# Kernel tuning notes

Measured on AMD Instinct MI355X. Metric: run time of the kernel, lower is better.

## Reference

```python
import jax, jax.numpy as jnp
import numpy as np

# ---- static config ----
B, D, H, W, C = 4, 8, 56, 56, 192
Md, Mh, Mw = 2, 7, 7
Sd, Sh, Sw = 1, 3, 3
NH = 6
HD = C // NH
SCALE = HD ** -0.5
N = Md * Mh * Mw  # 98
NW = (D // Md) * (H // Mh) * (W // Mw)  # 256 windows per batch element


def _rel_pos_index():
    coords = np.stack(np.meshgrid(np.arange(Md), np.arange(Mh), np.arange(Mw), indexing='ij'))
    cf = coords.reshape(3, -1)
    rc = (cf[:, :, None] - cf[:, None, :]).transpose(1, 2, 0)
    rc[..., 0] += Md - 1
    rc[..., 1] += Mh - 1
    rc[..., 2] += Mw - 1
    rc[..., 0] *= (2 * Mh - 1) * (2 * Mw - 1)
    rc[..., 1] *= 2 * Mw - 1
    return rc.sum(-1)  # (N, N) int

REL_IDX = jnp.asarray(_rel_pos_index())


def _build_attn_mask():
    img = np.zeros((D, H, W), dtype=np.float32)
    cnt = 0
    for ds in (slice(0, -Md), slice(-Md, -Sd), slice(-Sd, None)):
        for hs in (slice(0, -Mh), slice(-Mh, -Sh), slice(-Sh, None)):
            for ws in (slice(0, -Mw), slice(-Mw, -Sw), slice(-Sw, None)):
                img[ds, hs, ws] = cnt
                cnt += 1
    mw = img.reshape(D // Md, Md, H // Mh, Mh, W // Mw, Mw)
    mw = mw.transpose(0, 2, 4, 1, 3, 5).reshape(-1, N)  # (NW, N)
    am = mw[:, None, :] - mw[:, :, None]
    return np.where(am != 0, -100.0, 0.0).astype(np.float32)  # (NW, N, N)


def window_partition(x):  # (B, D, H, W, C) -> (B*NW, N, C)
    x = x.reshape(B, D // Md, Md, H // Mh, Mh, W // Mw, Mw, C)
    return x.transpose(0, 1, 3, 5, 2, 4, 6, 7).reshape(-1, N, C)


def window_reverse(w):  # (B*NW, N, C) -> (B, D, H, W, C)
    x = w.reshape(B, D // Md, H // Mh, W // Mw, Md, Mh, Mw, C)
    return x.transpose(0, 1, 4, 2, 5, 3, 6, 7).reshape(B, D, H, W, C)


def layer_norm(x, g, b, eps=1e-5):
    mu = x.mean(-1, keepdims=True)
    var = ((x - mu) ** 2).mean(-1, keepdims=True)
    return (x - mu) * jax.lax.rsqrt(var + eps) * g + b


def setup_inputs() -> dict:
    key = jax.random.key(0)
    ks = jax.random.split(key, 6)
    return {
        'x': jax.random.normal(ks[0], (B, D * H * W, C), jnp.float32),
        'attn_mask': jnp.asarray(_build_attn_mask()),
        'norm1_g': jnp.ones((C,), jnp.float32),
        'norm1_b': jnp.zeros((C,), jnp.float32),
        'qkv_w': jax.random.normal(ks[1], (3 * C, C), jnp.float32) * 0.02,
        'qkv_b': jnp.zeros((3 * C,), jnp.float32),
        'rel_bias': jax.random.normal(ks[2], ((2 * Md - 1) * (2 * Mh - 1) * (2 * Mw - 1), NH), jnp.float32) * 0.02,
        'proj_w': jax.random.normal(ks[3], (C, C), jnp.float32) * 0.02,
        'proj_b': jnp.zeros((C,), jnp.float32),
        'fc1_w': jax.random.normal(ks[4], (C, C), jnp.float32) * 0.02,
        'fc1_b': jnp.zeros((C,), jnp.float32),
    }


def reference(x, attn_mask, norm1_g, norm1_b, qkv_w, qkv_b, rel_bias, proj_w, proj_b, fc1_w, fc1_b):
    shortcut = x
    h = layer_norm(x, norm1_g, norm1_b).reshape(B, D, H, W, C)
    # cyclic shift (dims divisible by window -> no padding needed)
    h = jnp.roll(h, shift=(-Sd, -Sh, -Sw), axis=(1, 2, 3))
    xw = window_partition(h)  # (B*NW, N, C)
    B_ = xw.shape[0]
    qkv = (xw @ qkv_w.T + qkv_b).reshape(B_, N, 3, NH, HD).transpose(2, 0, 3, 1, 4)
    q, k, v = qkv[0], qkv[1], qkv[2]  # (B_, NH, N, HD)
    attn = jnp.einsum('bhnd,bhmd->bhnm', q * SCALE, k)
    bias = rel_bias[REL_IDX.reshape(-1)].reshape(N, N, NH).transpose(2, 0, 1)  # (NH, N, N)
    attn = attn + bias[None]
    # additive shift mask per window
    attn = attn.reshape(B, NW, NH, N, N) + attn_mask[None, :, None]
    attn = jax.nn.softmax(attn.reshape(B_, NH, N, N), axis=-1)
    out = jnp.einsum('bhnm,bhmd->bhnd', attn, v).transpose(0, 2, 1, 3).reshape(B_, N, C)
    out = out @ proj_w.T + proj_b
    h = window_reverse(out)
    h = jnp.roll(h, shift=(Sd, Sh, Sw), axis=(1, 2, 3)).reshape(B, D * H * W, C)
    h = jax.nn.gelu(h @ fc1_w.T + fc1_b, approximate=False)
    return shortcut + h
```

## Files before the change

### kernel.cpp

```cpp
#include <hip/hip_runtime.h>
#include <cstdint>
#include <cstddef>

typedef __bf16 bf16_t;
typedef __bf16 bf16x8 __attribute__((ext_vector_type(8)));
typedef float  f32x4  __attribute__((ext_vector_type(4)));

#define DHW   25088
#define SCALE 0.17677669529663687f

__device__ inline f32x4 mfma16(bf16x8 a, bf16x8 b, f32x4 c) {
  return __builtin_amdgcn_mfma_f32_16x16x32_bf16(a, b, c, 0, 0, 0);
}

__device__ inline size_t wrow_to_grow(int orow) {
  int win = orow / 98, tok = orow % 98;
  int b = win >> 8, wr = win & 255;
  int bd = wr >> 6, bh = (wr >> 3) & 7, bwi = wr & 7;
  int md = tok / 49, mh = (tok / 7) % 7, mw = tok % 7;
  int d = (bd * 2 + md + 1) & 7;
  int h = bh * 7 + mh + 3; if (h >= 56) h -= 56;
  int w = bwi * 7 + mw + 3; if (w >= 56) w -= 56;
  return (size_t)b * DHW + (size_t)((d * 56 + h) * 56 + w);
}

__global__ __launch_bounds__(256) void prep_all_kernel(
    const float* __restrict__ qkv_w, const float* __restrict__ proj_w,
    const float* __restrict__ fc1_w, const float* __restrict__ rel_bias,
    const float* __restrict__ mask,
    bf16_t* __restrict__ wq, bf16_t* __restrict__ wp, bf16_t* __restrict__ wf,
    bf16_t* __restrict__ bmr)
{
  int idx = blockIdx.x * 256 + threadIdx.x;
  if (idx < 110592) { wq[idx] = (bf16_t)qkv_w[idx]; return; }
  idx -= 110592;
  if (idx < 36864) { wp[idx] = (bf16_t)proj_w[idx]; return; }
  idx -= 36864;
  if (idx < 36864) { wf[idx] = (bf16_t)fc1_w[idx]; return; }
  idx -= 36864;
  if (idx >= 688128) return;
  int e    = idx & 31;
  int lane = (idx >> 5) & 63;
  int t2   = idx >> 11;
  int mt   = t2 % 7;
  int wh   = t2 / 7;
  int type = wh / 6, h = wh - type * 6;
  int winb = ((type & 4) ? 3 : 0) * 64 + ((type & 2) ? 7 : 0) * 8 + ((type & 1) ? 7 : 0);
  int g = lane >> 4, li = lane & 15;
  int nt2 = e >> 2, v = e & 3;
  int row = mt * 16 + g * 4 + v;
  int col = nt2 * 16 + li;
  float val = -1e30f;
  if (row < 98 && col < 98 && nt2 < 7) {
    int di = row / 49 - col / 49 + 1;
    int hi = (row / 7) % 7 - (col / 7) % 7 + 6;
    int wi = row % 7 - col % 7 + 6;
    int rid = di * 169 + hi * 13 + wi;
    val = mask[winb * 9604 + row * 98 + col] + rel_bias[rid * 6 + h];
  }
  bmr[idx] = (bf16_t)val;
}

__global__ __launch_bounds__(896) void fused_kernel(
    const float* __restrict__ x, const float* __restrict__ gw,
    const float* __restrict__ bw_, const bf16_t* __restrict__ wq,
    const float* __restrict__ qkv_b, const bf16_t* __restrict__ wp,
    const float* __restrict__ proj_b, const bf16_t* __restrict__ wf,
    const float* __restrict__ fc1_b, const bf16_t* __restrict__ bmr,
    float* __restrict__ out)
{
  __shared__ __align__(16) char smem[158528];
  bf16_t* U  = (bf16_t*)smem;
  bf16_t* Qs = (bf16_t*)(smem + 25600);
  bf16_t* Ks = (bf16_t*)(smem + 64800);
  bf16_t* Vt = (bf16_t*)(smem + 104000);
  float*  qb = (float*)(smem + 156224);
  float* gwb = (float*)smem;

  #define BS(r, c)     U[(r) * 200 + (c)]
  #define PSc(w, r, c) U[(w) * 640 + (r) * 40 + (c)]
  #define QS(r, c)     Qs[(r) * 200 + (c)]
  #define KS(r, c)     Ks[(r) * 200 + (c)]
  #define VT(d, t)     Vt[(d) * 136 + (t)]

  int win  = blockIdx.x;
  int winb = win & 255;
  int type = (((winb >> 6) == 3) ? 4 : 0) | ((((winb >> 3) & 7) == 7) ? 2 : 0)
           | (((winb & 7) == 7) ? 1 : 0);
  int tid  = threadIdx.x;
  int wid  = tid >> 6, lane = tid & 63;
  int wn = wid & 1, wm = wid >> 1;
  int g = lane >> 4, li = lane & 15;

  if (tid < 192) { gwb[tid] = gw[tid]; gwb[192 + tid] = bw_[tid]; }
  if (tid < 576) qb[tid] = qkv_b[tid];
  if (tid < 768) {
    uint4 z = {0u, 0u, 0u, 0u};
    int d = tid >> 2, part = tid & 3;
    *(uint4*)&VT(d, 96 + part * 8) = z;
  }

  int r = wm * 16 + li;
  float v[48];
  if (r < 98) {
    size_t growr = wrow_to_grow(win * 98 + r);
    const float* xr = x + growr * 192 + g * 8;
    #pragma unroll
    for (int ks = 0; ks < 6; ks++) {
      *(float4*)&v[ks * 8]     = *(const float4*)(xr + ks * 32);
      *(float4*)&v[ks * 8 + 4] = *(const float4*)(xr + ks * 32 + 4);
    }
  } else {
    #pragma unroll
    for (int i = 0; i < 48; i++) v[i] = 0.f;
  }
  float s = 0.f, sq = 0.f;
  #pragma unroll
  for (int i = 0; i < 48; i++) { s += v[i]; sq += v[i] * v[i]; }
  s += __shfl_xor(s, 16, 64); sq += __shfl_xor(sq, 16, 64);
  s += __shfl_xor(s, 32, 64); sq += __shfl_xor(sq, 32, 64);
  float mu   = s * (1.0f / 192.0f);
  float var  = sq * (1.0f / 192.0f) - mu * mu;
  float rstd = rsqrtf(var + 1e-5f);
  __syncthreads();
  bf16x8 afr[6];
  #pragma unroll
  for (int ks = 0; ks < 6; ks++) {
    bf16x8 t;
    #pragma unroll
    for (int j = 0; j < 8; j++) {
      int c = ks * 32 + g * 8 + j;
      t[j] = (r < 98) ? (bf16_t)((v[ks * 8 + j] - mu) * rstd * gwb[c] + gwb[192 + c])
                      : (bf16_t)0.0f;
    }
    afr[ks] = t;
  }

  uint4 st[2];
  #pragma unroll
  for (int i = 0; i < 2; i++) {
    int c = tid + 896 * i;
    if (c < 1536) {
      int rr = c / 24, ck = c % 24;
      st[i] = *(const uint4*)(wq + (size_t)rr * 192 + ck * 8);
    }
  }
  for (int nt = 0; nt < 9; nt++) {
    __syncthreads();
    #pragma unroll
    for (int i = 0; i < 2; i++) {
      int c = tid + 896 * i;
      if (c < 1536) {
        int rr = c / 24, ck = c % 24;
        *(uint4*)&BS(rr, ck * 8) = st[i];
      }
    }
    __syncthreads();
    if (nt < 8) {
      #pragma unroll
      for (int i = 0; i < 2; i++) {
        int c = tid + 896 * i;
        if (c < 1536) {
          int rr = c / 24, ck = c % 24;
          st[i] = *(const uint4*)(wq + (size_t)(nt + 1) * 12288 + (size_t)rr * 192 + ck * 8);
        }
      }
    }
    f32x4 acc[2] = {};
    #pragma unroll
    for (int ks = 0; ks < 6; ks++) {
      bf16x8 a = afr[ks];
      #pragma unroll
      for (int nl = 0; nl < 2; nl++) {
        bf16x8 b = *(const bf16x8*)&BS((wn * 2 + nl) * 16 + li, ks * 32 + g * 8);
        acc[nl] = mfma16(a, b, acc[nl]);
      }
    }
    #pragma unroll
    for (int nl = 0; nl < 2; nl++)
    #pragma unroll
    for (int vv = 0; vv < 4; vv++) {
      int row = wm * 16 + g * 4 + vv;
      if (row < 98) {
        int col = nt * 64 + (wn * 2 + nl) * 16 + li;
        float val = acc[nl][vv] + qb[col];
        if (nt < 3)      QS(row, col)       = (bf16_t)(val * SCALE);
        else if (nt < 6) KS(row, col - 192) = (bf16_t)val;
        else             VT(col - 384, row) = (bf16_t)val;
      }
    }
  }
  __syncthreads();

  int mt  = wm;
  int rq  = mt * 16 + li;
  int rqc = rq < 98 ? rq : 97;
  for (int hh = 0; hh < 3; hh++) {
    int h = wn * 3 + hh;
    const bf16_t* bmp = bmr + ((((size_t)(type * 6 + h)) * 7 + mt) * 64 + lane) * 32;
    bf16x8 bm0 = *(const bf16x8*)(bmp);
    bf16x8 bm1 = *(const bf16x8*)(bmp + 8);
    bf16x8 bm2 = *(const bf16x8*)(bmp + 16);
    bf16x8 bm3 = *(const bf16x8*)(bmp + 24);
    bf16x8 af = *(const bf16x8*)&QS(rqc, h * 32 + g * 8);
    float logit[7][4];
    #pragma unroll
    for (int nt2 = 0; nt2 < 7; nt2++) {
      int rk = nt2 * 16 + li;
      int rkc = rk < 98 ? rk : 97;
      bf16x8 bfr = *(const bf16x8*)&KS(rkc, h * 32 + g * 8);
      f32x4 z = {};
      f32x4 S = mfma16(af, bfr, z);
      #pragma unroll
      for (int vv = 0; vv < 4; vv++) {
        int e = nt2 * 4 + vv;
        float bmv = (e < 8) ? (float)bm0[e] : (e < 16) ? (float)bm1[e - 8]
                  : (e < 24) ? (float)bm2[e - 16] : (float)bm3[e - 24];
        logit[nt2][vv] = S[vv] + bmv;
      }
    }
    #pragma unroll
    for (int vv = 0; vv < 4; vv++) {
      float mx = logit[0][vv];
      #pragma unroll
      for (int nt2 = 1; nt2 < 7; nt2++) mx = fmaxf(mx, logit[nt2][vv]);
      #pragma unroll
      for (int off = 1; off < 16; off <<= 1) mx = fmaxf(mx, __shfl_xor(mx, off, 64));
      float se = 0.f;
      #pragma unroll
      for (int nt2 = 0; nt2 < 7; nt2++) {
        float p = __expf(logit[nt2][vv] - mx);
        logit[nt2][vv] = p; se += p;
      }
      #pragma unroll
      for (int off = 1; off < 16; off <<= 1) se += __shfl_xor(se, off, 64);
      float inv = 1.0f / se;
      #pragma unroll
      for (int nt2 = 0; nt2 < 7; nt2++) logit[nt2][vv] *= inv;
    }
    f32x4 o0 = {}, o1 = {};
    #pragma unroll
    for (int ch = 0; ch < 4; ch++) {
      #pragma unroll
      for (int nl = 0; nl < 2; nl++) {
        int nt2 = ch * 2 + nl;
        #pragma unroll
        for (int vv = 0; vv < 4; vv++) {
          bf16_t pv = (nt2 < 7) ? (bf16_t)logit[nt2][vv] : (bf16_t)0.0f;
          PSc(wid, g * 4 + vv, nl * 16 + li) = pv;
        }
      }
      bf16x8 pf = *(const bf16x8*)&PSc(wid, li, g * 8);
      bf16x8 v0 = *(const bf16x8*)&VT(h * 32 + li, ch * 32 + g * 8);
      bf16x8 v1 = *(const bf16x8*)&VT(h * 32 + 16 + li, ch * 32 + g * 8);
      o0 = mfma16(pf, v0, o0);
      o1 = mfma16(pf, v1, o1);
    }
    #pragma unroll
    for (int vv = 0; vv < 4; vv++) {
      int row = mt * 16 + g * 4 + vv;
      if (row < 98) {
        QS(row, h * 32 + li)      = (bf16_t)o0[vv];
        QS(row, h * 32 + 16 + li) = (bf16_t)o1[vv];
      }
    }
  }
  __syncthreads();

  float* bfb = qb;
  if (tid < 192) bfb[tid] = proj_b[tid];
  bf16x8 a2[6];
  #pragma unroll
  for (int ks = 0; ks < 6; ks++)
    a2[ks] = *(const bf16x8*)&QS(rqc, ks * 32 + g * 8);
  #pragma unroll
  for (int i = 0; i < 2; i++) {
    int c = tid + 896 * i;
    if (c < 1536) {
      int rr = c / 24, ck = c % 24;
      st[i] = *(const uint4*)(wp + (size_t)rr * 192 + ck * 8);
    }
  }
  for (int nt = 0; nt < 3; nt++) {
    __syncthreads();
    #pragma unroll
    for (int i = 0; i < 2; i++) {
      int c = tid + 896 * i;
      if (c < 1536) {
        int rr = c / 24, ck = c % 24;
        *(uint4*)&BS(rr, ck * 8) = st[i];
      }
    }
    __syncthreads();
    if (nt < 2) {
      #pragma unroll
      for (int i = 0; i < 2; i++) {
        int c = tid + 896 * i;
        if (c < 1536) {
          int rr = c / 24, ck = c % 24;
          st[i] = *(const uint4*)(wp + (size_t)(nt + 1) * 12288 + (size_t)rr * 192 + ck * 8);
        }
      }
    }
    f32x4 acc[2] = {};
    #pragma unroll
    for (int ks = 0; ks < 6; ks++) {
      bf16x8 a = a2[ks];
      #pragma unroll
      for (int nl = 0; nl < 2; nl++) {
        bf16x8 b = *(const bf16x8*)&BS((wn * 2 + nl) * 16 + li, ks * 32 + g * 8);
        acc[nl] = mfma16(a, b, acc[nl]);
      }
    }
    #pragma unroll
    for (int nl = 0; nl < 2; nl++)
    #pragma unroll
    for (int vv = 0; vv < 4; vv++) {
      int row = wm * 16 + g * 4 + vv;
      if (row < 98) {
        int col = nt * 64 + (wn * 2 + nl) * 16 + li;
        KS(row, col) = (bf16_t)(acc[nl][vv] + bfb[col]);
      }
    }
  }
  __syncthreads();

  if (tid < 192) bfb[tid] = fc1_b[tid];
  bf16x8 a3[6];
  #pragma unroll
  for (int ks = 0; ks < 6; ks++)
    a3[ks] = *(const bf16x8*)&KS(rqc, ks * 32 + g * 8);
  #pragma unroll
  for (int i = 0; i < 2; i++) {
    int c = tid + 896 * i;
    if (c < 1536) {
      int rr = c / 24, ck = c % 24;
      st[i] = *(const uint4*)(wf + (size_t)rr * 192 + ck * 8);
    }
  }
  size_t growv[4];
  #pragma unroll
  for (int vv = 0; vv < 4; vv++) {
    int row = wm * 16 + g * 4 + vv;
    growv[vv] = (row < 98) ? wrow_to_grow(win * 98 + row) : (size_t)0;
  }
  for (int nt = 0; nt < 3; nt++) {
    __syncthreads();
    #pragma unroll
    for (int i = 0; i < 2; i++) {
      int c = tid + 896 * i;
      if (c < 1536) {
        int rr = c / 24, ck = c % 24;
        *(uint4*)&BS(rr, ck * 8) = st[i];
      }
    }
    __syncthreads();
    if (nt < 2) {
      #pragma unroll
      for (int i = 0; i < 2; i++) {
        int c = tid + 896 * i;
        if (c < 1536) {
          int rr = c / 24, ck = c % 24;
          st[i] = *(const uint4*)(wf + (size_t)(nt + 1) * 12288 + (size_t)rr * 192 + ck * 8);
        }
      }
    }
    f32x4 acc[2] = {};
    #pragma unroll
    for (int ks = 0; ks < 6; ks++) {
      bf16x8 a = a3[ks];
      #pragma unroll
      for (int nl = 0; nl < 2; nl++) {
        bf16x8 b = *(const bf16x8*)&BS((wn * 2 + nl) * 16 + li, ks * 32 + g * 8);
        acc[nl] = mfma16(a, b, acc[nl]);
      }
    }
    #pragma unroll
    for (int vv = 0; vv < 4; vv++) {
      int row = wm * 16 + g * 4 + vv;
      if (row < 98) {
        const float* xr = x + growv[vv] * 192;
        float* op = out + growv[vv] * 192;
        #pragma unroll
        for (int nl = 0; nl < 2; nl++) {
          int col = nt * 64 + (wn * 2 + nl) * 16 + li;
          float val = acc[nl][vv] + bfb[col];
          float ge = 0.5f * val * (1.0f + erff(val * 0.70710678118654752f));
          op[col] = xr[col] + ge;
        }
      }
    }
  }
  #undef BS
  #undef PSc
  #undef QS
  #undef KS
  #undef VT
}

extern "C" void kernel_launch(void* const* d_in, const int* in_sizes, int n_in,
                              void* d_out, int out_size, void* d_ws, size_t ws_size,
                              hipStream_t stream) {
  (void)in_sizes; (void)n_in; (void)out_size; (void)ws_size;
  const float* x         = (const float*)d_in[0];
  const float* attn_mask = (const float*)d_in[1];
  const float* n1g       = (const float*)d_in[2];
  const float* n1b       = (const float*)d_in[3];
  const float* qkv_w     = (const float*)d_in[4];
  const float* qkv_b     = (const float*)d_in[5];
  const float* rel_bias  = (const float*)d_in[6];
  const float* proj_w    = (const float*)d_in[7];
  const float* proj_b    = (const float*)d_in[8];
  const float* fc1_w     = (const float*)d_in[9];
  const float* fc1_b     = (const float*)d_in[10];
  float* out = (float*)d_out;

  char* ws = (char*)d_ws;
  size_t off = 0;
  auto alloc = [&](size_t bytes) -> char* {
    char* p = ws + off;
    off += (bytes + 255) & ~(size_t)255;
    return p;
  };
  bf16_t* wq  = (bf16_t*)alloc(110592 * 2);
  bf16_t* wp  = (bf16_t*)alloc(36864 * 2);
  bf16_t* wf  = (bf16_t*)alloc(36864 * 2);
  bf16_t* bmr = (bf16_t*)alloc((size_t)688128 * 2);

  prep_all_kernel<<<3408, 256, 0, stream>>>(qkv_w, proj_w, fc1_w, rel_bias,
                                            attn_mask, wq, wp, wf, bmr);
  fused_kernel<<<1024, 896, 0, stream>>>(x, n1g, n1b, wq, qkv_b, wp, proj_b,
                                         wf, fc1_b, bmr, out);
}
```

Measured before the change: 387.0 us.

## Interleave QKV projection with per-head-pair attention to shrink LDS footprint

Restructures the fused Swin block kernel so that QKV is computed two heads at a time, with attention run for that pair right after, instead of materializing full Q/K/V for all heads. Shared memory drops from about 158KB to about 79KB, which could allow two workgroups per CU. Register pressure is also lowered: LayerNorm inputs are re-read from global rather than held in 48 registers, logits are packed as fp16 pairs, and launch bounds gain a minimum-occupancy hint. The costs are recomputing the LayerNorm fragments three times, extra syncs per head pair, and fp16 rounding of logits before softmax.

```diff
diff --git a/kernel.cpp b/kernel.cpp
--- a/kernel.cpp
+++ b/kernel.cpp
@@ -4,13 +4,27 @@
 
 typedef __bf16 bf16_t;
 typedef __bf16 bf16x8 __attribute__((ext_vector_type(8)));
+typedef __bf16 bf16x4 __attribute__((ext_vector_type(4)));
 typedef float  f32x4  __attribute__((ext_vector_type(4)));
+typedef _Float16 f16_t;
 
 #define DHW   25088
 #define SCALE 0.17677669529663687f
 
 __device__ inline f32x4 mfma16(bf16x8 a, bf16x8 b, f32x4 c) {
   return __builtin_amdgcn_mfma_f32_16x16x32_bf16(a, b, c, 0, 0, 0);
+}
+
+__device__ inline unsigned pkh(float a, float b) {
+  unsigned short ua = __builtin_bit_cast(unsigned short, (f16_t)a);
+  unsigned short ub = __builtin_bit_cast(unsigned short, (f16_t)b);
+  return (unsigned)ua | ((unsigned)ub << 16);
+}
+__device__ inline float upklo(unsigned u) {
+  return (float)__builtin_bit_cast(f16_t, (unsigned short)(u & 0xffffu));
+}
+__device__ inline float upkhi(unsigned u) {
+  return (float)__builtin_bit_cast(f16_t, (unsigned short)(u >> 16));
 }
 
 __device__ inline size_t wrow_to_grow(int orow) {
@@ -61,7 +75,7 @@
   bmr[idx] = (bf16_t)val;
 }
 
-__global__ __launch_bounds__(896) void fused_kernel(
+__global__ __launch_bounds__(896, 7) void fused_kernel(
     const float* __restrict__ x, const float* __restrict__ gw,
     const float* __restrict__ bw_, const bf16_t* __restrict__ wq,
     const float* __restrict__ qkv_b, const bf16_t* __restrict__ wp,
@@ -69,19 +83,22 @@
     const float* __restrict__ fc1_b, const bf16_t* __restrict__ bmr,
     float* __restrict__ out)
 {
-  __shared__ __align__(16) char smem[158528];
-  bf16_t* U  = (bf16_t*)smem;
-  bf16_t* Qs = (bf16_t*)(smem + 25600);
-  bf16_t* Ks = (bf16_t*)(smem + 64800);
-  bf16_t* Vt = (bf16_t*)(smem + 104000);
-  float*  qb = (float*)(smem + 156224);
-  float* gwb = (float*)smem;
+  __shared__ __align__(16) char smem[79104];
+  bf16_t* U   = (bf16_t*)smem;
+  bf16_t* Qh  = (bf16_t*)(smem + 25600);
+  bf16_t* Kh  = (bf16_t*)(smem + 41728);
+  bf16_t* Vt  = (bf16_t*)(smem + 57856);
+  bf16_t* AoS = (bf16_t*)(smem + 25600);
+  bf16_t* C1  = (bf16_t*)(smem + 25600);
+  float*  qb  = (float*)(smem + 75264);
+  float*  gwb = (float*)(smem + 77568);
 
   #define BS(r, c)     U[(r) * 200 + (c)]
   #define PSc(w, r, c) U[(w) * 640 + (r) * 40 + (c)]
-  #define QS(r, c)     Qs[(r) * 200 + (c)]
-  #define KS(r, c)     Ks[(r) * 200 + (c)]
+  #define QH(r, c)     Qh[(r) * 72 + (c)]
+  #define KH(r, c)     Kh[(r) * 72 + (c)]
   #define VT(d, t)     Vt[(d) * 136 + (t)]
+  #define C1M(r, c)    C1[(r) * 200 + (c)]
 
   int win  = blockIdx.x;
   int winb = win & 255;
@@ -94,59 +111,76 @@
 
   if (tid < 192) { gwb[tid] = gw[tid]; gwb[192 + tid] = bw_[tid]; }
   if (tid < 576) qb[tid] = qkv_b[tid];
-  if (tid < 768) {
+  {
     uint4 z = {0u, 0u, 0u, 0u};
-    int d = tid >> 2, part = tid & 3;
-    *(uint4*)&VT(d, 96 + part * 8) = z;
+    for (int c = tid; c < 1088; c += 896) ((uint4*)Vt)[c] = z;
   }
 
   int r = wm * 16 + li;
-  float v[48];
+  const float* xr = nullptr;
   if (r < 98) {
     size_t growr = wrow_to_grow(win * 98 + r);
-    const float* xr = x + growr * 192 + g * 8;
+    xr = x + growr * 192 + g * 8;
+  }
+  float mu, rstd;
+  {
+    float s = 0.f, sq = 0.f;
+    if (xr) {
+      #pragma unroll
+      for (int ks = 0; ks < 6; ks++) {
+        float4 a = *(const float4*)(xr + ks * 32);
+        float4 b = *(const float4*)(xr + ks * 32 + 4);
+        s += a.x + a.y + a.z + a.w + b.x + b.y + b.z + b.w;
+        sq += a.x*a.x + a.y*a.y + a.z*a.z + a.w*a.w
+            + b.x*b.x + b.y*b.y + b.z*b.z + b.w*b.w;
+      }
+    }
+    s += __shfl_xor(s, 16, 64); sq += __shfl_xor(sq, 16, 64);
+    s += __shfl_xor(s, 32, 64); sq += __shfl_xor(sq, 32, 64);
+    mu = s * (1.0f / 192.0f);
+    float var = sq * (1.0f / 192.0f) - mu * mu;
+    rstd = rsqrtf(var + 1e-5f);
+  }
+  __syncthreads();
+
+  auto build_afr = [&](bf16x8* afr) {
     #pragma unroll
     for (int ks = 0; ks < 6; ks++) {
-      *(float4*)&v[ks * 8]     = *(const float4*)(xr + ks * 32);
-      *(float4*)&v[ks * 8 + 4] = *(const float4*)(xr + ks * 32 + 4);
-    }
-  } else {
-    #pragma unroll
-    for (int i = 0; i < 48; i++) v[i] = 0.f;
-  }
-  float s = 0.f, sq = 0.f;
-  #pragma unroll
-  for (int i = 0; i < 48; i++) { s += v[i]; sq += v[i] * v[i]; }
-  s += __shfl_xor(s, 16, 64); sq += __shfl_xor(sq, 16, 64);
-  s += __shfl_xor(s, 32, 64); sq += __shfl_xor(sq, 32, 64);
-  float mu   = s * (1.0f / 192.0f);
-  float var  = sq * (1.0f / 192.0f) - mu * mu;
-  float rstd = rsqrtf(var + 1e-5f);
-  __syncthreads();
-  bf16x8 afr[6];
-  #pragma unroll
-  for (int ks = 0; ks < 6; ks++) {
-    bf16x8 t;
-    #pragma unroll
-    for (int j = 0; j < 8; j++) {
-      int c = ks * 32 + g * 8 + j;
-      t[j] = (r < 98) ? (bf16_t)((v[ks * 8 + j] - mu) * rstd * gwb[c] + gwb[192 + c])
-                      : (bf16_t)0.0f;
-    }
-    afr[ks] = t;
-  }
+      bf16x8 t;
+      if (xr) {
+        int c0 = ks * 32 + g * 8;
+        float4 a = *(const float4*)(xr + ks * 32);
+        float4 b = *(const float4*)(xr + ks * 32 + 4);
+        float4 ga = *(const float4*)&gwb[c0],      gb = *(const float4*)&gwb[c0 + 4];
+        float4 ba = *(const float4*)&gwb[192 + c0], bb = *(const float4*)&gwb[192 + c0 + 4];
+        t[0] = (bf16_t)((a.x - mu) * rstd * ga.x + ba.x);
+        t[1] = (bf16_t)((a.y - mu) * rstd * ga.y + ba.y);
+        t[2] = (bf16_t)((a.z - mu) * rstd * ga.z + ba.z);
+        t[3] = (bf16_t)((a.w - mu) * rstd * ga.w + ba.w);
+        t[4] = (bf16_t)((b.x - mu) * rstd * gb.x + bb.x);
+        t[5] = (bf16_t)((b.y - mu) * rstd * gb.y + bb.y);
+        t[6] = (bf16_t)((b.z - mu) * rstd * gb.z + bb.z);
+        t[7] = (bf16_t)((b.w - mu) * rstd * gb.w + bb.w);
+      } else {
+        #pragma unroll
+        for (int j = 0; j < 8; j++) t[j] = (bf16_t)0.0f;
+      }
+      afr[ks] = t;
+    }
+  };
 
   uint4 st[2];
-  #pragma unroll
-  for (int i = 0; i < 2; i++) {
-    int c = tid + 896 * i;
-    if (c < 1536) {
-      int rr = c / 24, ck = c % 24;
-      st[i] = *(const uint4*)(wq + (size_t)rr * 192 + ck * 8);
-    }
-  }
-  for (int nt = 0; nt < 9; nt++) {
-    __syncthreads();
+  auto loadw = [&](const bf16_t* w, int tile) {
+    #pragma unroll
+    for (int i = 0; i < 2; i++) {
+      int c = tid + 896 * i;
+      if (c < 1536) {
+        int rr = c / 24, ck = c % 24;
+        st[i] = *(const uint4*)(w + (size_t)tile * 12288 + (size_t)rr * 192 + ck * 8);
+      }
+    }
+  };
+  auto storebs = [&]() {
     #pragma unroll
     for (int i = 0; i < 2; i++) {
       int c = tid + 896 * i;
@@ -155,26 +189,154 @@
         *(uint4*)&BS(rr, ck * 8) = st[i];
       }
     }
+  };
+
+  int rqc = (wm * 16 + li < 98) ? (wm * 16 + li) : 97;
+  bf16x8 a2loc[3];
+
+  loadw(wq, 0);
+  #pragma unroll
+  for (int hp = 0; hp < 3; hp++) {
+    bf16x8 afr[6];
+    build_afr(afr);
+    for (int tp = 0; tp < 3; tp++) {
+      __syncthreads();
+      storebs();
+      __syncthreads();
+      if (tp < 2) loadw(wq, hp + 3 * (tp + 1));
+      f32x4 acc[2] = {};
+      #pragma unroll
+      for (int ks = 0; ks < 6; ks++) {
+        bf16x8 b0 = *(const bf16x8*)&BS((wn * 2 + 0) * 16 + li, ks * 32 + g * 8);
+        bf16x8 b1 = *(const bf16x8*)&BS((wn * 2 + 1) * 16 + li, ks * 32 + g * 8);
+        acc[0] = mfma16(afr[ks], b0, acc[0]);
+        acc[1] = mfma16(afr[ks], b1, acc[1]);
+      }
+      #pragma unroll
+      for (int nl = 0; nl < 2; nl++)
+      #pragma unroll
+      for (int vv = 0; vv < 4; vv++) {
+        int row = wm * 16 + g * 4 + vv;
+        if (row < 98) {
+          int cl = (wn * 2 + nl) * 16 + li;
+          float val = acc[nl][vv] + qb[tp * 192 + hp * 64 + cl];
+          if (tp == 0)      QH(row, cl) = (bf16_t)(val * SCALE);
+          else if (tp == 1) KH(row, cl) = (bf16_t)val;
+          else              VT(cl, row) = (bf16_t)val;
+        }
+      }
+    }
     __syncthreads();
-    if (nt < 8) {
-      #pragma unroll
-      for (int i = 0; i < 2; i++) {
-        int c = tid + 896 * i;
-        if (c < 1536) {
-          int rr = c / 24, ck = c % 24;
-          st[i] = *(const uint4*)(wq + (size_t)(nt + 1) * 12288 + (size_t)rr * 192 + ck * 8);
+
+    {
+      int h = 2 * hp + wn, hl = wn * 32;
+      const bf16_t* bmp = bmr + ((((size_t)(type * 6 + h)) * 7 + wm) * 64 + lane) * 32;
+      bf16x8 af = *(const bf16x8*)&QH(rqc, hl + g * 8);
+      unsigned lp[7][2];
+      float mx0 = -3.0e38f, mx1 = -3.0e38f, mx2 = -3.0e38f, mx3 = -3.0e38f;
+      #pragma unroll
+      for (int nt2 = 0; nt2 < 7; nt2++) {
+        int rk = nt2 * 16 + li;
+        int rkc = rk < 98 ? rk : 97;
+        bf16x8 kf = *(const bf16x8*)&KH(rkc, hl + g * 8);
+        f32x4 z = {};
+        f32x4 S = mfma16(af, kf, z);
+        bf16x4 bm4 = *(const bf16x4*)(bmp + nt2 * 4);
+        float l0 = S[0] + (float)bm4[0];
+        float l1 = S[1] + (float)bm4[1];
+        float l2 = S[2] + (float)bm4[2];
+        float l3 = S[3] + (float)bm4[3];
+        mx0 = fmaxf(mx0, l0); mx1 = fmaxf(mx1, l1);
+        mx2 = fmaxf(mx2, l2); mx3 = fmaxf(mx3, l3);
+        lp[nt2][0] = pkh(l0, l1);
+        lp[nt2][1] = pkh(l2, l3);
+      }
+      #pragma unroll
+      for (int off = 1; off < 16; off <<= 1) {
+        mx0 = fmaxf(mx0, __shfl_xor(mx0, off, 64));
+        mx1 = fmaxf(mx1, __shfl_xor(mx1, off, 64));
+        mx2 = fmaxf(mx2, __shfl_xor(mx2, off, 64));
+        mx3 = fmaxf(mx3, __shfl_xor(mx3, off, 64));
+      }
+      float se0 = 0.f, se1 = 0.f, se2 = 0.f, se3 = 0.f;
+      #pragma unroll
+      for (int nt2 = 0; nt2 < 7; nt2++) {
+        float p0 = __expf(upklo(lp[nt2][0]) - mx0);
+        float p1 = __expf(upkhi(lp[nt2][0]) - mx1);
+        float p2 = __expf(upklo(lp[nt2][1]) - mx2);
+        float p3 = __expf(upkhi(lp[nt2][1]) - mx3);
+        se0 += p0; se1 += p1; se2 += p2; se3 += p3;
+        lp[nt2][0] = pkh(p0, p1);
+        lp[nt2][1] = pkh(p2, p3);
+      }
+      #pragma unroll
+      for (int off = 1; off < 16; off <<= 1) {
+        se0 += __shfl_xor(se0, off, 64); se1 += __shfl_xor(se1, off, 64);
+        se2 += __shfl_xor(se2, off, 64); se3 += __shfl_xor(se3, off, 64);
+      }
+      float inv0 = 1.0f / se0, inv1 = 1.0f / se1;
+      float inv2 = 1.0f / se2, inv3 = 1.0f / se3;
+      f32x4 o0 = {}, o1 = {};
+      #pragma unroll
+      for (int ch = 0; ch < 4; ch++) {
+        #pragma unroll
+        for (int nl = 0; nl < 2; nl++) {
+          int nt2 = ch * 2 + nl;
+          if (nt2 < 7) {
+            PSc(wid, g * 4 + 0, nl * 16 + li) = (bf16_t)(upklo(lp[nt2][0]) * inv0);
+            PSc(wid, g * 4 + 1, nl * 16 + li) = (bf16_t)(upkhi(lp[nt2][0]) * inv1);
+            PSc(wid, g * 4 + 2, nl * 16 + li) = (bf16_t)(upklo(lp[nt2][1]) * inv2);
+            PSc(wid, g * 4 + 3, nl * 16 + li) = (bf16_t)(upkhi(lp[nt2][1]) * inv3);
+          } else {
+            PSc(wid, g * 4 + 0, nl * 16 + li) = (bf16_t)0.0f;
+            PSc(wid, g * 4 + 1, nl * 16 + li) = (bf16_t)0.0f;
+            PSc(wid, g * 4 + 2, nl * 16 + li) = (bf16_t)0.0f;
+            PSc(wid, g * 4 + 3, nl * 16 + li) = (bf16_t)0.0f;
+          }
         }
-      }
-    }
+        bf16x8 pf = *(const bf16x8*)&PSc(wid, li, g * 8);
+        bf16x8 v0 = *(const bf16x8*)&VT(hl + li, ch * 32 + g * 8);
+        bf16x8 v1 = *(const bf16x8*)&VT(hl + 16 + li, ch * 32 + g * 8);
+        o0 = mfma16(pf, v0, o0);
+        o1 = mfma16(pf, v1, o1);
+      }
+      #pragma unroll
+      for (int vv = 0; vv < 4; vv++) {
+        PSc(wid, g * 4 + vv, li)      = (bf16_t)o0[vv];
+        PSc(wid, g * 4 + vv, 16 + li) = (bf16_t)o1[vv];
+      }
+      a2loc[hp] = *(const bf16x8*)&PSc(wid, li, g * 8);
+    }
+    if (hp < 2) loadw(wq, hp + 1);
+    else        loadw(wp, 0);
+  }
+
+  __syncthreads();
+  #pragma unroll
+  for (int hp = 0; hp < 3; hp++) {
+    int ks = 2 * hp + wn;
+    *(bf16x8*)(AoS + (size_t)(wm * 6 + ks) * 512 + lane * 8) = a2loc[hp];
+  }
+  if (tid < 192) qb[tid] = proj_b[tid];
+  __syncthreads();
+  bf16x8 a2[6];
+  #pragma unroll
+  for (int ks = 0; ks < 6; ks++)
+    a2[ks] = *(const bf16x8*)(AoS + (size_t)(wm * 6 + ks) * 512 + lane * 8);
+
+  for (int tp = 0; tp < 3; tp++) {
+    __syncthreads();
+    storebs();
+    __syncthreads();
+    if (tp < 2) loadw(wp, tp + 1);
+    else        loadw(wf, 0);
     f32x4 acc[2] = {};
     #pragma unroll
     for (int ks = 0; ks < 6; ks++) {
-      bf16x8 a = afr[ks];
-      #pragma unroll
-      for (int nl = 0; nl < 2; nl++) {
-        bf16x8 b = *(const bf16x8*)&BS((wn * 2 + nl) * 16 + li, ks * 32 + g * 8);
-        acc[nl] = mfma16(a, b, acc[nl]);
-      }
+      bf16x8 b0 = *(const bf16x8*)&BS((wn * 2 + 0) * 16 + li, ks * 32 + g * 8);
+      bf16x8 b1 = *(const bf16x8*)&BS((wn * 2 + 1) * 16 + li, ks * 32 + g * 8);
+      acc[0] = mfma16(a2[ks], b0, acc[0]);
+      acc[1] = mfma16(a2[ks], b1, acc[1]);
     }
     #pragma unroll
     for (int nl = 0; nl < 2; nl++)
@@ -182,220 +344,60 @@
     for (int vv = 0; vv < 4; vv++) {
       int row = wm * 16 + g * 4 + vv;
       if (row < 98) {
-        int col = nt * 64 + (wn * 2 + nl) * 16 + li;
-        float val = acc[nl][vv] + qb[col];
-        if (nt < 3)      QS(row, col)       = (bf16_t)(val * SCALE);
-        else if (nt < 6) KS(row, col - 192) = (bf16_t)val;
-        else             VT(col - 384, row) = (bf16_t)val;
+        int cl = tp * 64 + (wn * 2 + nl) * 16 + li;
+        C1M(row, cl) = (bf16_t)(acc[nl][vv] + qb[cl]);
       }
     }
   }
   __syncthreads();
 
-  int mt  = wm;
-  int rq  = mt * 16 + li;
-  int rqc = rq < 98 ? rq : 97;
-  for (int hh = 0; hh < 3; hh++) {
-    int h = wn * 3 + hh;
-    const bf16_t* bmp = bmr + ((((size_t)(type * 6 + h)) * 7 + mt) * 64 + lane) * 32;
-    bf16x8 bm0 = *(const bf16x8*)(bmp);
-    bf16x8 bm1 = *(const bf16x8*)(bmp + 8);
-    bf16x8 bm2 = *(const bf16x8*)(bmp + 16);
-    bf16x8 bm3 = *(const bf16x8*)(bmp + 24);
-    bf16x8 af = *(const bf16x8*)&QS(rqc, h * 32 + g * 8);
-    float logit[7][4];
-    #pragma unroll
-    for (int nt2 = 0; nt2 < 7; nt2++) {
-      int rk = nt2 * 16 + li;
-      int rkc = rk < 98 ? rk : 97;
-      bf16x8 bfr = *(const bf16x8*)&KS(rkc, h * 32 + g * 8);
-      f32x4 z = {};
-      f32x4 S = mfma16(af, bfr, z);
-      #pragma unroll
-      for (int vv = 0; vv < 4; vv++) {
-        int e = nt2 * 4 + vv;
-        float bmv = (e < 8) ? (float)bm0[e] : (e < 16) ? (float)bm1[e - 8]
-                  : (e < 24) ? (float)bm2[e - 16] : (float)bm3[e - 24];
-        logit[nt2][vv] = S[vv] + bmv;
-      }
-    }
-    #pragma unroll
-    for (int vv = 0; vv < 4; vv++) {
-      float mx = logit[0][vv];
-      #pragma unroll
-      for (int nt2 = 1; nt2 < 7; nt2++) mx = fmaxf(mx, logit[nt2][vv]);
-      #pragma unroll
-      for (int off = 1; off < 16; off <<= 1) mx = fmaxf(mx, __shfl_xor(mx, off, 64));
-      float se = 0.f;
-      #pragma unroll
-      for (int nt2 = 0; nt2 < 7; nt2++) {
-        float p = __expf(logit[nt2][vv] - mx);
-        logit[nt2][vv] = p; se += p;
-      }
-      #pragma unroll
-      for (int off = 1; off < 16; off <<= 1) se += __shfl_xor(se, off, 64);
-      float inv = 1.0f / se;
-      #pragma unroll
-      for (int nt2 = 0; nt2 < 7; nt2++) logit[nt2][vv] *= inv;
-    }
-    f32x4 o0 = {}, o1 = {};
-    #pragma unroll
-    for (int ch = 0; ch < 4; ch++) {
-      #pragma unroll
-      for (int nl = 0; nl < 2; nl++) {
-        int nt2 = ch * 2 + nl;
-        #pragma unroll
-        for (int vv = 0; vv < 4; vv++) {
-          bf16_t pv = (nt2 < 7) ? (bf16_t)logit[nt2][vv] : (bf16_t)0.0f;
-          PSc(wid, g * 4 + vv, nl * 16 + li) = pv;
-        }
-      }
-      bf16x8 pf = *(const bf16x8*)&PSc(wid, li, g * 8);
-      bf16x8 v0 = *(const bf16x8*)&VT(h * 32 + li, ch * 32 + g * 8);
-      bf16x8 v1 = *(const bf16x8*)&VT(h * 32 + 16 + li, ch * 32 + g * 8);
-      o0 = mfma16(pf, v0, o0);
-      o1 = mfma16(pf, v1, o1);
-    }
-    #pragma unroll
-    for (int vv = 0; vv < 4; vv++) {
-      int row = mt * 16 + g * 4 + vv;
-      if (row < 98) {
-        QS(row, h * 32 + li)      = (bf16_t)o0[vv];
-        QS(row, h * 32 + 16 + li) = (bf16_t)o1[vv];
-      }
-    }
-  }
-  __syncthreads();
-
-  float* bfb = qb;
-  if (tid < 192) bfb[tid] = proj_b[tid];
-  bf16x8 a2[6];
-  #pragma unroll
-  for (int ks = 0; ks < 6; ks++)
-    a2[ks] = *(const bf16x8*)&QS(rqc, ks * 32 + g * 8);
-  #pragma unroll
-  for (int i = 0; i < 2; i++) {
-    int c = tid + 896 * i;
-    if (c < 1536) {
-      int rr = c / 24, ck = c % 24;
-      st[i] = *(const uint4*)(wp + (size_t)rr * 192 + ck * 8);
-    }
-  }
-  for (int nt = 0; nt < 3; nt++) {
-    __syncthreads();
-    #pragma unroll
-    for (int i = 0; i < 2; i++) {
-      int c = tid + 896 * i;
-      if (c < 1536) {
-        int rr = c / 24, ck = c % 24;
-        *(uint4*)&BS(rr, ck * 8) = st[i];
-      }
-    }
-    __syncthreads();
-    if (nt < 2) {
-      #pragma unroll
-      for (int i = 0; i < 2; i++) {
-        int c = tid + 896 * i;
-        if (c < 1536) {
-          int rr = c / 24, ck = c % 24;
-          st[i] = *(const uint4*)(wp + (size_t)(nt + 1) * 12288 + (size_t)rr * 192 + ck * 8);
-        }
-      }
-    }
-    f32x4 acc[2] = {};
-    #pragma unroll
-    for (int ks = 0; ks < 6; ks++) {
-      bf16x8 a = a2[ks];
-      #pragma unroll
-      for (int nl = 0; nl < 2; nl++) {
-        bf16x8 b = *(const bf16x8*)&BS((wn * 2 + nl) * 16 + li, ks * 32 + g * 8);
-        acc[nl] = mfma16(a, b, acc[nl]);
-      }
-    }
-    #pragma unroll
-    for (int nl = 0; nl < 2; nl++)
-    #pragma unroll
-    for (int vv = 0; vv < 4; vv++) {
-      int row = wm * 16 + g * 4 + vv;
-      if (row < 98) {
-        int col = nt * 64 + (wn * 2 + nl) * 16 + li;
-        KS(row, col) = (bf16_t)(acc[nl][vv] + bfb[col]);
-      }
-    }
-  }
-  __syncthreads();
-
-  if (tid < 192) bfb[tid] = fc1_b[tid];
   bf16x8 a3[6];
   #pragma unroll
   for (int ks = 0; ks < 6; ks++)
-    a3[ks] = *(const bf16x8*)&KS(rqc, ks * 32 + g * 8);
-  #pragma unroll
-  for (int i = 0; i < 2; i++) {
-    int c = tid + 896 * i;
-    if (c < 1536) {
-      int rr = c / 24, ck = c % 24;
-      st[i] = *(const uint4*)(wf + (size_t)rr * 192 + ck * 8);
-    }
-  }
+    a3[ks] = *(const bf16x8*)&C1M(rqc, ks * 32 + g * 8);
+  if (tid < 192) qb[tid] = fc1_b[tid];
   size_t growv[4];
   #pragma unroll
   for (int vv = 0; vv < 4; vv++) {
     int row = wm * 16 + g * 4 + vv;
     growv[vv] = (row < 98) ? wrow_to_grow(win * 98 + row) : (size_t)0;
   }
-  for (int nt = 0; nt < 3; nt++) {
+
+  for (int tp = 0; tp < 3; tp++) {
     __syncthreads();
-    #pragma unroll
-    for (int i = 0; i < 2; i++) {
-      int c = tid + 896 * i;
-      if (c < 1536) {
-        int rr = c / 24, ck = c % 24;
-        *(uint4*)&BS(rr, ck * 8) = st[i];
-      }
-    }
+    storebs();
     __syncthreads();
-    if (nt < 2) {
-      #pragma unroll
-      for (int i = 0; i < 2; i++) {
-        int c = tid + 896 * i;
-        if (c < 1536) {
-          int rr = c / 24, ck = c % 24;
-          st[i] = *(const uint4*)(wf + (size_t)(nt + 1) * 12288 + (size_t)rr * 192 + ck * 8);
-        }
-      }
-    }
+    if (tp < 2) loadw(wf, tp + 1);
     f32x4 acc[2] = {};
     #pragma unroll
     for (int ks = 0; ks < 6; ks++) {
-      bf16x8 a = a3[ks];
-      #pragma unroll
-      for (int nl = 0; nl < 2; nl++) {
-        bf16x8 b = *(const bf16x8*)&BS((wn * 2 + nl) * 16 + li, ks * 32 + g * 8);
-        acc[nl] = mfma16(a, b, acc[nl]);
-      }
+      bf16x8 b0 = *(const bf16x8*)&BS((wn * 2 + 0) * 16 + li, ks * 32 + g * 8);
+      bf16x8 b1 = *(const bf16x8*)&BS((wn * 2 + 1) * 16 + li, ks * 32 + g * 8);
+      acc[0] = mfma16(a3[ks], b0, acc[0]);
+      acc[1] = mfma16(a3[ks], b1, acc[1]);
     }
     #pragma unroll
     for (int vv = 0; vv < 4; vv++) {
       int row = wm * 16 + g * 4 + vv;
       if (row < 98) {
-        const float* xr = x + growv[vv] * 192;
+        const float* xrr = x + growv[vv] * 192;
         float* op = out + growv[vv] * 192;
         #pragma unroll
         for (int nl = 0; nl < 2; nl++) {
-          int col = nt * 64 + (wn * 2 + nl) * 16 + li;
-          float val = acc[nl][vv] + bfb[col];
+          int cl = tp * 64 + (wn * 2 + nl) * 16 + li;
+          float val = acc[nl][vv] + qb[cl];
           float ge = 0.5f * val * (1.0f + erff(val * 0.70710678118654752f));
-          op[col] = xr[col] + ge;
+          op[cl] = xrr[cl] + ge;
         }
       }
     }
   }
   #undef BS
   #undef PSc
-  #undef QS
-  #undef KS
+  #undef QH
+  #undef KH
   #undef VT
+  #undef C1M
 }
 
 extern "C" void kernel_launch(void* const* d_in, const int* in_sizes, int n_in,
```

Result: slower. 507.8 us (+31.2%).

## Load GEMM weight fragments directly from global memory instead of staging through LDS

Applied to the files above, without the earlier changes.

The QKV, proj and fc1 GEMMs no longer copy 64-row weight tiles into shared memory behind two __syncthreads per tile. Each wave now reads its B fragments straight from global memory, relying on L2/L1 because every block reads the same small weights. The proj and fc1 biases are preloaded into dedicated LDS buffers at kernel start, so the barriers before those GEMMs are no longer needed for bias staging. This removes many barriers and LDS round-trips and shrinks LDS use, but it exposes global-load latency inside the MFMA loops with no prefetch, and the 7 row-waves issue redundant loads of the same weights.

```diff
diff --git a/kernel.cpp b/kernel.cpp
--- a/kernel.cpp
+++ b/kernel.cpp
@@ -69,15 +69,16 @@
     const float* __restrict__ fc1_b, const bf16_t* __restrict__ bmr,
     float* __restrict__ out)
 {
-  __shared__ __align__(16) char smem[158528];
+  __shared__ __align__(16) char smem[152384];
   bf16_t* U  = (bf16_t*)smem;
-  bf16_t* Qs = (bf16_t*)(smem + 25600);
-  bf16_t* Ks = (bf16_t*)(smem + 64800);
-  bf16_t* Vt = (bf16_t*)(smem + 104000);
-  float*  qb = (float*)(smem + 156224);
+  bf16_t* Qs = (bf16_t*)(smem + 17920);
+  bf16_t* Ks = (bf16_t*)(smem + 57120);
+  bf16_t* Vt = (bf16_t*)(smem + 96320);
+  float*  qb = (float*)(smem + 148544);
+  float*  pbuf = (float*)(smem + 150848);
+  float*  fbuf = (float*)(smem + 151616);
   float* gwb = (float*)smem;
 
-  #define BS(r, c)     U[(r) * 200 + (c)]
   #define PSc(w, r, c) U[(w) * 640 + (r) * 40 + (c)]
   #define QS(r, c)     Qs[(r) * 200 + (c)]
   #define KS(r, c)     Ks[(r) * 200 + (c)]
@@ -94,6 +95,9 @@
 
   if (tid < 192) { gwb[tid] = gw[tid]; gwb[192 + tid] = bw_[tid]; }
   if (tid < 576) qb[tid] = qkv_b[tid];
+  if (tid >= 576 && tid < 768) pbuf[tid - 576] = proj_b[tid - 576];
+  if (tid >= 768 && tid < 896) fbuf[tid - 768] = fc1_b[tid - 768];
+  if (tid < 64) fbuf[128 + tid] = fc1_b[128 + tid];
   if (tid < 768) {
     uint4 z = {0u, 0u, 0u, 0u};
     int d = tid >> 2, part = tid & 3;
@@ -136,45 +140,16 @@
     afr[ks] = t;
   }
 
-  uint4 st[2];
-  #pragma unroll
-  for (int i = 0; i < 2; i++) {
-    int c = tid + 896 * i;
-    if (c < 1536) {
-      int rr = c / 24, ck = c % 24;
-      st[i] = *(const uint4*)(wq + (size_t)rr * 192 + ck * 8);
-    }
-  }
   for (int nt = 0; nt < 9; nt++) {
-    __syncthreads();
-    #pragma unroll
-    for (int i = 0; i < 2; i++) {
-      int c = tid + 896 * i;
-      if (c < 1536) {
-        int rr = c / 24, ck = c % 24;
-        *(uint4*)&BS(rr, ck * 8) = st[i];
-      }
-    }
-    __syncthreads();
-    if (nt < 8) {
-      #pragma unroll
-      for (int i = 0; i < 2; i++) {
-        int c = tid + 896 * i;
-        if (c < 1536) {
-          int rr = c / 24, ck = c % 24;
-          st[i] = *(const uint4*)(wq + (size_t)(nt + 1) * 12288 + (size_t)rr * 192 + ck * 8);
-        }
-      }
-    }
+    const bf16_t* bp0 = wq + ((size_t)nt * 64 + (wn * 2 + 0) * 16 + li) * 192 + g * 8;
+    const bf16_t* bp1 = bp0 + 16 * 192;
     f32x4 acc[2] = {};
     #pragma unroll
     for (int ks = 0; ks < 6; ks++) {
-      bf16x8 a = afr[ks];
-      #pragma unroll
-      for (int nl = 0; nl < 2; nl++) {
-        bf16x8 b = *(const bf16x8*)&BS((wn * 2 + nl) * 16 + li, ks * 32 + g * 8);
-        acc[nl] = mfma16(a, b, acc[nl]);
-      }
+      bf16x8 b0 = *(const bf16x8*)(bp0 + ks * 32);
+      bf16x8 b1 = *(const bf16x8*)(bp1 + ks * 32);
+      acc[0] = mfma16(afr[ks], b0, acc[0]);
+      acc[1] = mfma16(afr[ks], b1, acc[1]);
     }
     #pragma unroll
     for (int nl = 0; nl < 2; nl++)
@@ -267,50 +242,20 @@
   }
   __syncthreads();
 
-  float* bfb = qb;
-  if (tid < 192) bfb[tid] = proj_b[tid];
   bf16x8 a2[6];
   #pragma unroll
   for (int ks = 0; ks < 6; ks++)
     a2[ks] = *(const bf16x8*)&QS(rqc, ks * 32 + g * 8);
-  #pragma unroll
-  for (int i = 0; i < 2; i++) {
-    int c = tid + 896 * i;
-    if (c < 1536) {
-      int rr = c / 24, ck = c % 24;
-      st[i] = *(const uint4*)(wp + (size_t)rr * 192 + ck * 8);
-    }
-  }
   for (int nt = 0; nt < 3; nt++) {
-    __syncthreads();
-    #pragma unroll
-    for (int i = 0; i < 2; i++) {
-      int c = tid + 896 * i;
-      if (c < 1536) {
-        int rr = c / 24, ck = c % 24;
-        *(uint4*)&BS(rr, ck * 8) = st[i];
-      }
-    }
-    __syncthreads();
-    if (nt < 2) {
-      #pragma unroll
-      for (int i = 0; i < 2; i++) {
-        int c = tid + 896 * i;
-        if (c < 1536) {
-          int rr = c / 24, ck = c % 24;
-          st[i] = *(const uint4*)(wp + (size_t)(nt + 1) * 12288 + (size_t)rr * 192 + ck * 8);
-        }
-      }
-    }
+    const bf16_t* bp0 = wp + ((size_t)nt * 64 + (wn * 2 + 0) * 16 + li) * 192 + g * 8;
+    const bf16_t* bp1 = bp0 + 16 * 192;
     f32x4 acc[2] = {};
     #pragma unroll
     for (int ks = 0; ks < 6; ks++) {
-      bf16x8 a = a2[ks];
-      #pragma unroll
-      for (int nl = 0; nl < 2; nl++) {
-        bf16x8 b = *(const bf16x8*)&BS((wn * 2 + nl) * 16 + li, ks * 32 + g * 8);
-        acc[nl] = mfma16(a, b, acc[nl]);
-      }
+      bf16x8 b0 = *(const bf16x8*)(bp0 + ks * 32);
+      bf16x8 b1 = *(const bf16x8*)(bp1 + ks * 32);
+      acc[0] = mfma16(a2[ks], b0, acc[0]);
+      acc[1] = mfma16(a2[ks], b1, acc[1]);
     }
     #pragma unroll
     for (int nl = 0; nl < 2; nl++)
@@ -319,25 +264,16 @@
       int row = wm * 16 + g * 4 + vv;
       if (row < 98) {
         int col = nt * 64 + (wn * 2 + nl) * 16 + li;
-        KS(row, col) = (bf16_t)(acc[nl][vv] + bfb[col]);
+        KS(row, col) = (bf16_t)(acc[nl][vv] + pbuf[col]);
       }
     }
   }
   __syncthreads();
 
-  if (tid < 192) bfb[tid] = fc1_b[tid];
   bf16x8 a3[6];
   #pragma unroll
   for (int ks = 0; ks < 6; ks++)
     a3[ks] = *(const bf16x8*)&KS(rqc, ks * 32 + g * 8);
-  #pragma unroll
-  for (int i = 0; i < 2; i++) {
-    int c = tid + 896 * i;
-    if (c < 1536) {
-      int rr = c / 24, ck = c % 24;
-      st[i] = *(const uint4*)(wf + (size_t)rr * 192 + ck * 8);
-    }
-  }
   size_t growv[4];
   #pragma unroll
   for (int vv = 0; vv < 4; vv++) {
@@ -345,53 +281,32 @@
     growv[vv] = (row < 98) ? wrow_to_grow(win * 98 + row) : (size_t)0;
   }
   for (int nt = 0; nt < 3; nt++) {
-    __syncthreads();
-    #pragma unroll
-    for (int i = 0; i < 2; i++) {
-      int c = tid + 896 * i;
-      if (c < 1536) {
-        int rr = c / 24, ck = c % 24;
-        *(uint4*)&BS(rr, ck * 8) = st[i];
-      }
-    }
-    __syncthreads();
-    if (nt < 2) {
-      #pragma unroll
-      for (int i = 0; i < 2; i++) {
-        int c = tid + 896 * i;
-        if (c < 1536) {
-          int rr = c / 24, ck = c % 24;
-          st[i] = *(const uint4*)(wf + (size_t)(nt + 1) * 12288 + (size_t)rr * 192 + ck * 8);
-        }
-      }
-    }
+    const bf16_t* bp0 = wf + ((size_t)nt * 64 + (wn * 2 + 0) * 16 + li) * 192 + g * 8;
+    const bf16_t* bp1 = bp0 + 16 * 192;
     f32x4 acc[2] = {};
     #pragma unroll
     for (int ks = 0; ks < 6; ks++) {
-      bf16x8 a = a3[ks];
-      #pragma unroll
-      for (int nl = 0; nl < 2; nl++) {
-        bf16x8 b = *(const bf16x8*)&BS((wn * 2 + nl) * 16 + li, ks * 32 + g * 8);
-        acc[nl] = mfma16(a, b, acc[nl]);
-      }
+      bf16x8 b0 = *(const bf16x8*)(bp0 + ks * 32);
+      bf16x8 b1 = *(const bf16x8*)(bp1 + ks * 32);
+      acc[0] = mfma16(a3[ks], b0, acc[0]);
+      acc[1] = mfma16(a3[ks], b1, acc[1]);
     }
     #pragma unroll
     for (int vv = 0; vv < 4; vv++) {
       int row = wm * 16 + g * 4 + vv;
       if (row < 98) {
-        const float* xr = x + growv[vv] * 192;
+        const float* xrr = x + growv[vv] * 192;
         float* op = out + growv[vv] * 192;
         #pragma unroll
         for (int nl = 0; nl < 2; nl++) {
           int col = nt * 64 + (wn * 2 + nl) * 16 + li;
-          float val = acc[nl][vv] + bfb[col];
+          float val = acc[nl][vv] + fbuf[col];
           float ge = 0.5f * val * (1.0f + erff(val * 0.70710678118654752f));
-          op[col] = xr[col] + ge;
+          op[col] = xrr[col] + ge;
         }
       }
     }
   }
-  #undef BS
   #undef PSc
   #undef QS
   #undef KS
```

Result: slower. 513.6 us (+32.7%).
